# Optimization experiments

Measured on AMD Instinct MI355X. Metric: run time of the kernel, lower is better.

The kernel has to match this reference:

```python
import jax, jax.numpy as jnp
import numpy as np

NEG_SLOPE = 0.2
EPS = 1e-16  # PyG softmax eps


def gat_layer(x, edge_index, W_lin, b_lin, W_attn, b_attn):
    # GATConv: add self loops, x = lin(x), per-edge attention, segment softmax over
    # target nodes (edge_index[1]), scatter-add of x_j * alpha.
    N = x.shape[0]
    loops = jnp.arange(N, dtype=edge_index.dtype)
    src = jnp.concatenate([edge_index[0], loops])  # j (source / neighbor)
    dst = jnp.concatenate([edge_index[1], loops])  # i (target)
    x = x @ W_lin.T + b_lin                        # [N, D]
    D = x.shape[1]
    xi = x[dst]                                    # [E, D]
    xj = x[src]                                    # [E, D]
    # attn(cat(x_i, x_j)) split to avoid materializing the [E, 2D] concat
    Wi, Wj = W_attn[:, :D], W_attn[:, D:]
    alpha = xi @ Wi.T + xj @ Wj.T + b_attn         # [E, D]
    alpha = jax.nn.leaky_relu(alpha, NEG_SLOPE)
    # numerically stable segment softmax grouped by dst (per output channel)
    m = jax.ops.segment_max(alpha, dst, num_segments=N)
    alpha = jnp.exp(alpha - m[dst])
    denom = jax.ops.segment_sum(alpha, dst, num_segments=N)
    alpha = alpha / (denom[dst] + EPS)
    return jax.ops.segment_sum(xj * alpha, dst, num_segments=N)


def setup_inputs() -> dict:
    key = jax.random.key(0)
    ks = jax.random.split(key, 22)
    B, L, NN, E = 64, 50, 500, 256000
    EMB, D = 128, 128
    N = B * NN
    w = lambda k, shape: jax.random.normal(k, shape, jnp.float32) * 0.05
    return {
        "x": jax.random.normal(ks[0], (N, EMB), jnp.float32),
        "edge_index_0": jax.random.randint(ks[1], (2, E), 0, N, jnp.int32),
        "edge_index_1": jax.random.randint(ks[2], (2, E), 0, N, jnp.int32),
        "state_": jax.random.normal(ks[3], (B, D), jnp.float32),
        "input_": jax.random.normal(ks[4], (B, L, EMB), jnp.float32),
        "W_in": w(ks[5], (D, EMB)),
        "W_z": w(ks[6], (D, 2 * D)),
        "W_r": w(ks[7], (D, 2 * D)),
        "W_h": w(ks[8], (D, 2 * D)),
        "g0_Wlin": w(ks[9], (D, EMB)),
        "g0_blin": w(ks[10], (D,)),
        "g0_Wattn": w(ks[11], (D, 2 * D)),
        "g0_battn": w(ks[12], (D,)),
        "g1_Wlin": w(ks[13], (D, D)),
        "g1_blin": w(ks[14], (D,)),
        "g1_Wattn": w(ks[15], (D, 2 * D)),
        "g1_battn": w(ks[16], (D,)),
        "Wp": w(ks[17], (1, D)),
        "bp": w(ks[18], (1,)),
        "Ws": w(ks[19], (1, D)),
        "bs": w(ks[20], (1,)),
    }


def reference(x, edge_index_0, edge_index_1, state_, input_,
              W_in, W_z, W_r, W_h,
              g0_Wlin, g0_blin, g0_Wattn, g0_battn,
              g1_Wlin, g1_blin, g1_Wattn, g1_battn,
              Wp, bp, Ws, bs):
    B, D = state_.shape
    n_nodes = x.shape[0] // B
    # GRU-style gate on global state
    inp = jnp.mean(input_ @ W_in.T, axis=1)                 # [B, D]
    zi = jnp.concatenate([state_, inp], axis=-1)            # [B, 2D]
    z = jax.nn.sigmoid(zi @ W_z.T)
    r = jax.nn.sigmoid(zi @ W_r.T)
    h = jnp.tanh(jnp.concatenate([r * state_, inp], -1) @ W_h.T)
    h = (1 - z) * state_ + z * h                            # [B, D]
    # two GAT layers
    g0 = gat_layer(x, edge_index_0, g0_Wlin, g0_blin, g0_Wattn, g0_battn)
    g1 = gat_layer(g0, edge_index_1, g1_Wlin, g1_blin, g1_Wattn, g1_battn)
    xg = g1.reshape(B, n_nodes, D) * h[:, None, :]          # broadcast gate
    prob = (xg @ Wp.T + bp).reshape(B, n_nodes)
    sisr = jax.nn.sigmoid((xg @ Ws.T + bs).reshape(B, n_nodes))
    prob = jax.nn.softmax(prob[:, 1:], axis=-1)             # drop depot node 0
    return prob, sisr, h
```

## Files before the change

### kernel.cpp

```cpp
#include <hip/hip_runtime.h>
#include <math.h>

#define CAP  32
#define CAPB 4096
#define PART_CHUNK 4096

typedef __attribute__((ext_vector_type(8))) short bfrag;
typedef __attribute__((ext_vector_type(4))) float ffrag;
typedef __attribute__((ext_vector_type(2))) float f2v;

__device__ __forceinline__ float sigmoidf_(float x){ return 1.f/(1.f+__expf(-x)); }

__device__ __forceinline__ unsigned short f2bf(float f){
    unsigned u = __float_as_uint(f);
    u += 0x7fffu + ((u >> 16) & 1u);
    return (unsigned short)(u >> 16);
}
__device__ __forceinline__ float bf2f(unsigned u){
    return __uint_as_float((u & 0xffffu) << 16);
}

__global__ __launch_bounds__(256) void prep_kernel(
    const int* __restrict__ ei0, const int* __restrict__ ei1,
    int* __restrict__ binCnt, unsigned* __restrict__ bins, int E, int nA, int nb,
    const float* __restrict__ Wlin0, const float* __restrict__ Wattn0,
    const float* __restrict__ blin0, const float* __restrict__ battn0,
    const float* __restrict__ Wlin1, const float* __restrict__ Wattn1,
    const float* __restrict__ blin1, const float* __restrict__ battn1,
    unsigned short* __restrict__ wc, float* __restrict__ bc,
    const float* __restrict__ state_, const float* __restrict__ input_,
    const float* __restrict__ W_in, const float* __restrict__ W_z,
    const float* __restrict__ W_r, const float* __restrict__ W_h,
    float* __restrict__ h_out, int L)
{
    int blk = blockIdx.x;
    if (blk < 2 * nA) {
        __shared__ int lcnt[128];
        __shared__ int gbase[128];
        int g = (blk >= nA) ? 1 : 0;
        const int* ei = g ? ei1 : ei0;
        int base = (blk - g * nA) * PART_CHUNK;
        int tid = threadIdx.x;
        for (int t = tid; t < nb; t += 256) lcnt[t] = 0;
        __syncthreads();
        int lpos[16], binv[16]; unsigned wrd[16];
        #pragma unroll
        for (int i = 0; i < 16; ++i) {
            int e = base + i * 256 + tid;
            if (e < E) {
                int d = ei[E + e];
                int s = ei[e];
                int b = d >> 8;
                binv[i] = b;
                wrd[i]  = ((unsigned)(d & 255) << 24) | (unsigned)s;
                lpos[i] = atomicAdd(&lcnt[b], 1);
            } else binv[i] = -1;
        }
        __syncthreads();
        if (tid < nb) gbase[tid] = atomicAdd(&binCnt[g * nb + tid], lcnt[tid]);
        __syncthreads();
        #pragma unroll
        for (int i = 0; i < 16; ++i) {
            if (binv[i] >= 0) {
                int pos = gbase[binv[i]] + lpos[i];
                if (pos < CAPB) bins[(size_t)(g * nb + binv[i]) * CAPB + pos] = wrd[i];
            }
        }
    } else if (blk < 2 * nA + 387) {
        int idx = (blk - 2 * nA) * 256 + threadIdx.x;
        if (idx < 2 * 384 * 128) {
            int layer = idx / 49152;
            int t = idx - layer * 49152;
            int n = t >> 7, k = t & 127;
            const float* Wlin  = layer ? Wlin1  : Wlin0;
            const float* Wattn = layer ? Wattn1 : Wattn0;
            float v;
            if (n < 128) {
                v = Wlin[n * 128 + k];
            } else {
                int rr = (n < 256) ? (n - 128) : (n - 256);
                int off = (n < 256) ? 0 : 128;
                float s = 0.f;
                for (int d = 0; d < 128; ++d) s += Wattn[rr * 256 + off + d] * Wlin[d * 128 + k];
                v = s;
            }
            wc[idx] = f2bf(v);
        } else if (idx < 2 * 384 * 128 + 768) {
            int bi = idx - 2 * 384 * 128;
            int layer = bi / 384;
            int n = bi - layer * 384;
            const float* blin  = layer ? blin1  : blin0;
            const float* Wattn = layer ? Wattn1 : Wattn0;
            const float* battn = layer ? battn1 : battn0;
            float v;
            if (n < 128) v = blin[n];
            else {
                int rr = (n < 256) ? (n - 128) : (n - 256);
                int off = (n < 256) ? 0 : 128;
                float s = 0.f;
                for (int d = 0; d < 128; ++d) s += Wattn[rr * 256 + off + d] * blin[d];
                v = (n < 256) ? (s + battn[rr]) : s;
            }
            bc[bi] = v;
        }
    } else {
        __shared__ float wt[128 * 65];
        __shared__ float mu[128], ziv[256], zi2[256], zzv[128], stv[128];
        int tid = threadIdx.x;
        int b = blk - (2 * nA + 387);

        if (tid < 128) {
            float s = 0.f;
            const float* ip = input_ + (size_t)b * L * 128 + tid;
            #pragma unroll 5
            for (int l = 0; l < L; ++l) s += ip[(size_t)l * 128];
            mu[tid] = s / (float)L;
            float st = state_[b * 128 + tid];
            stv[tid] = st;
            ziv[tid] = st;
        }
        __syncthreads();

        #define LOADTILE(W, ldk, k0) { \
            _Pragma("unroll") \
            for (int j = 0; j < 8; ++j) { \
                int f = tid + 256 * j;                  \
                int row = f >> 4, c4 = (f & 15) << 2; \
                float4 v = *(const float4*)((W) + (size_t)row * (ldk) + (k0) + c4); \
                float* wp = &wt[row * 65 + c4]; \
                wp[0] = v.x; wp[1] = v.y; wp[2] = v.z; wp[3] = v.w; \
            } }
        #define GEMVT(vec, k0, acc) { \
            if (tid < 128) { \
                const float* wr_ = &wt[tid * 65]; \
                _Pragma("unroll") \
                for (int c = 0; c < 64; ++c) acc += wr_[c] * (vec)[(k0) + c]; \
            } }

        float accI = 0.f;
        LOADTILE(W_in, 128, 0);  __syncthreads(); GEMVT(mu, 0, accI);  __syncthreads();
        LOADTILE(W_in, 128, 64); __syncthreads(); GEMVT(mu, 64, accI); __syncthreads();
        if (tid < 128) ziv[128 + tid] = accI;
        __syncthreads();

        float accZ = 0.f;
        #pragma unroll
        for (int t4 = 0; t4 < 4; ++t4) {
            LOADTILE(W_z, 256, t4 * 64); __syncthreads();
            GEMVT(ziv, t4 * 64, accZ);   __syncthreads();
        }
        float accR = 0.f;
        #pragma unroll
        for (int t4 = 0; t4 < 4; ++t4) {
            LOADTILE(W_r, 256, t4 * 64); __syncthreads();
            GEMVT(ziv, t4 * 64, accR);   __syncthreads();
        }
        if (tid < 128) {
            float z = sigmoidf_(accZ), r = sigmoidf_(accR);
            zzv[tid] = z;
            zi2[tid] = r * stv[tid];
            zi2[128 + tid] = ziv[128 + tid];
        }
        __syncthreads();
        float accH = 0.f;
        #pragma unroll
        for (int t4 = 0; t4 < 4; ++t4) {
            LOADTILE(W_h, 256, t4 * 64); __syncthreads();
            GEMVT(zi2, t4 * 64, accH);   __syncthreads();
        }
        if (tid < 128) {
            float hc = tanhf(accH);
            float z = zzv[tid], st = stv[tid];
            h_out[b * 128 + tid] = (1.f - z) * st + z * hc;
        }
        #undef LOADTILE
        #undef GEMVT
    }
}

__global__ __launch_bounds__(256) void gemm384(const short* __restrict__ Xb, const float* __restrict__ Xf,
                                               const short* __restrict__ Wc, const float* __restrict__ bc,
                                               unsigned short* __restrict__ aib, unsigned short* __restrict__ pair,
                                               const unsigned* __restrict__ bins, const int* __restrict__ binCnt,
                                               int* __restrict__ cnt, unsigned short* __restrict__ esrc,
                                               int N, int nb, int gemmBlks)
{
    __shared__ __align__(16) char smem[384 * 40 * 2];
    if ((int)blockIdx.x >= gemmBlks) {
        int* cl = (int*)smem;
        unsigned short* el = (unsigned short*)(smem + 1024);
        int p = blockIdx.x - gemmBlks;
        int g = (p >= nb) ? 1 : 0;
        int bin = p - g * nb;
        int tid = threadIdx.x;
        cl[tid] = 0;
        __syncthreads();
        int m = binCnt[g * nb + bin]; if (m > CAPB) m = CAPB;
        const unsigned* bp_ = bins + (size_t)(g * nb + bin) * CAPB;
        for (int i = tid; i < m; i += 256) {
            unsigned w = bp_[i];
            int dl = (int)(w >> 24);
            int pp = atomicAdd(&cl[dl], 1);
            if (pp < CAP) el[dl * CAP + pp] = (unsigned short)w;
        }
        __syncthreads();
        int nodeBase = bin * 256;
        int* cg = cnt + (size_t)g * N;
        if (nodeBase + tid < N) cg[nodeBase + tid] = cl[tid];
        uint4* eo = (uint4*)(esrc + ((size_t)g * N + nodeBase) * CAP);
        const uint4* es = (const uint4*)el;
        #pragma unroll
        for (int k = 0; k < 4; ++k) eo[k * 256 + tid] = es[k * 256 + tid];
        return;
    }
    short* wlds = (short*)smem;
    int tid = threadIdx.x;
    int lane = tid & 63, wave = tid >> 6;
    int quad = lane >> 4, l16 = lane & 15;
    int mrow = blockIdx.x * 64 + wave * 16 + l16;

    bfrag av[4];
    if (Xf) {
        #pragma unroll
        for (int kk = 0; kk < 4; ++kk) {
            const float* xfp = Xf + (size_t)mrow * 128 + quad * 8 + kk * 32;
            float4 a0 = *(const float4*)(xfp);
            float4 a1 = *(const float4*)(xfp + 4);
            av[kk] = (bfrag){ (short)f2bf(a0.x), (short)f2bf(a0.y), (short)f2bf(a0.z), (short)f2bf(a0.w),
                              (short)f2bf(a1.x), (short)f2bf(a1.y), (short)f2bf(a1.z), (short)f2bf(a1.w) };
        }
    } else {
        #pragma unroll
        for (int kk = 0; kk < 4; ++kk)
            av[kk] = *(const bfrag*)(Xb + (size_t)mrow * 128 + quad * 8 + kk * 32);
    }

    ffrag acc[24];
    #pragma unroll
    for (int t = 0; t < 24; ++t) acc[t] = (ffrag){0.f, 0.f, 0.f, 0.f};

    #pragma unroll
    for (int kk = 0; kk < 4; ++kk) {
        __syncthreads();
        #pragma unroll
        for (int it = 0; it < 6; ++it) {
            int slot = it * 256 + tid;
            int row = slot >> 2, ch = slot & 3;
            *(bfrag*)&wlds[row * 40 + ch * 8] = *(const bfrag*)(Wc + (size_t)row * 128 + kk * 32 + ch * 8);
        }
        __syncthreads();
        #pragma unroll
        for (int t = 0; t < 24; ++t) {
            bfrag bv = *(const bfrag*)&wlds[(t * 16 + l16) * 40 + quad * 8];
            acc[t] = __builtin_amdgcn_mfma_f32_16x16x32_bf16(av[kk], bv, acc[t], 0, 0, 0);
        }
    }
    int rbase = blockIdx.x * 64 + wave * 16 + quad * 4;
    #pragma unroll
    for (int t = 0; t < 8; ++t) {
        int c = t * 16 + l16;
        float by = bc[c], bi = bc[128 + c], bj = bc[256 + c];
        #pragma unroll
        for (int r = 0; r < 4; ++r) {
            size_t off = (size_t)(rbase + r) * 128 + c;
            float yv  = acc[t][r]      + by;
            float aiv = acc[8 + t][r]  + bi;
            float ajv = acc[16 + t][r] + bj;
            aib[off] = f2bf(aiv);
            int w = __builtin_amdgcn_cvt_pk_fp8_f32(yv, ajv, 0, false);
            pair[off] = (unsigned short)w;
        }
    }
}

__global__ void aggregate_kernel(const unsigned short* __restrict__ aib, const unsigned* __restrict__ pair,
                                 const int* __restrict__ cnt, const unsigned short* __restrict__ esrc,
                                 unsigned* __restrict__ gb_out,
                                 const float* __restrict__ h, const float* __restrict__ Wp, const float* __restrict__ bp,
                                 const float* __restrict__ Ws, const float* __restrict__ bs,
                                 float* __restrict__ pbuf, float* __restrict__ sisr_out,
                                 int N, int NN, int fuse_score)
{
    int node = blockIdx.x * (blockDim.x >> 6) + (threadIdx.x >> 6);
    if (node >= N) return;
    int lane = threadIdx.x & 63;
    int c = 2 * lane;
    unsigned ain2 = *(const unsigned*)(aib + ((size_t)node << 7) + c);
    float ain0 = bf2f(ain2), ain1 = bf2f(ain2 >> 16);
    int deg = cnt[node]; if (deg > CAP) deg = CAP;
    const unsigned short* ep = esrc + (size_t)node * CAP;
    int myidx = (lane < deg) ? (int)ep[lane] : 0;

    float w0 = 0.f, w1 = 0.f, o0 = 0.f, o1 = 0.f;
    #define PROC(q) { \
        f2v lo = __builtin_amdgcn_cvt_pk_f32_fp8((int)(q), false); \
        f2v hi = __builtin_amdgcn_cvt_pk_f32_fp8((int)(q), true); \
        float a0 = ain0 + lo.y; \
        float a1 = ain1 + hi.y; \
        a0 = (a0 > 0.f) ? a0 : 0.2f * a0; \
        a1 = (a1 > 0.f) ? a1 : 0.2f * a1; \
        float e0 = __expf(a0), e1 = __expf(a1); \
        w0 += e0; w1 += e1; \
        o0 += e0 * lo.x; o1 += e1 * hi.x; }

    unsigned qs = pair[((size_t)node << 6) + lane];
    PROC(qs)

    int j = 0;
    for (; j + 8 <= deg; j += 8) {
        int s0 = __shfl(myidx, j),     s1 = __shfl(myidx, j + 1);
        int s2 = __shfl(myidx, j + 2), s3 = __shfl(myidx, j + 3);
        int s4 = __shfl(myidx, j + 4), s5 = __shfl(myidx, j + 5);
        int s6 = __shfl(myidx, j + 6), s7 = __shfl(myidx, j + 7);
        unsigned q0 = pair[((size_t)s0 << 6) + lane];
        unsigned q1 = pair[((size_t)s1 << 6) + lane];
        unsigned q2 = pair[((size_t)s2 << 6) + lane];
        unsigned q3 = pair[((size_t)s3 << 6) + lane];
        unsigned q4 = pair[((size_t)s4 << 6) + lane];
        unsigned q5 = pair[((size_t)s5 << 6) + lane];
        unsigned q6 = pair[((size_t)s6 << 6) + lane];
        unsigned q7 = pair[((size_t)s7 << 6) + lane];
        PROC(q0) PROC(q1) PROC(q2) PROC(q3) PROC(q4) PROC(q5) PROC(q6) PROC(q7)
    }
    if (j + 4 <= deg) {
        int s0 = __shfl(myidx, j),     s1 = __shfl(myidx, j + 1);
        int s2 = __shfl(myidx, j + 2), s3 = __shfl(myidx, j + 3);
        unsigned q0 = pair[((size_t)s0 << 6) + lane];
        unsigned q1 = pair[((size_t)s1 << 6) + lane];
        unsigned q2 = pair[((size_t)s2 << 6) + lane];
        unsigned q3 = pair[((size_t)s3 << 6) + lane];
        PROC(q0) PROC(q1) PROC(q2) PROC(q3)
        j += 4;
    }
    for (; j < deg; ++j) {
        int s0 = __shfl(myidx, j);
        unsigned q0 = pair[((size_t)s0 << 6) + lane];
        PROC(q0)
    }
    #undef PROC

    float g0 = o0 / (w0 + 1e-16f), g1 = o1 / (w1 + 1e-16f);
    if (!fuse_score) {
        gb_out[(size_t)node * 64 + lane] = (unsigned)f2bf(g0) | ((unsigned)f2bf(g1) << 16);
    } else {
        int b = node / NN;
        float xg0 = g0 * h[b * 128 + c], xg1 = g1 * h[b * 128 + c + 1];
        float pp = xg0 * Wp[c] + xg1 * Wp[c + 1];
        float ss = xg0 * Ws[c] + xg1 * Ws[c + 1];
        #pragma unroll
        for (int o = 32; o > 0; o >>= 1) { pp += __shfl_xor(pp, o); ss += __shfl_xor(ss, o); }
        if (lane == 0) {
            pbuf[node] = pp + bp[0];
            sisr_out[node] = sigmoidf_(ss + bs[0]);
        }
    }
}

__global__ void softmax_kernel(const float* __restrict__ pbuf, float* __restrict__ prob_out, int NN){
    int b = blockIdx.x, tid = threadIdx.x;
    __shared__ float sdata[512];
    bool valid = (tid >= 1 && tid < NN);
    float v = valid ? pbuf[b * NN + tid] : -INFINITY;
    sdata[tid] = v; __syncthreads();
    for (int o = 256; o > 0; o >>= 1) { if (tid < o) sdata[tid] = fmaxf(sdata[tid], sdata[tid + o]); __syncthreads(); }
    float m = sdata[0]; __syncthreads();
    float e = valid ? __expf(v - m) : 0.f;
    sdata[tid] = e; __syncthreads();
    for (int o = 256; o > 0; o >>= 1) { if (tid < o) sdata[tid] += sdata[tid + o]; __syncthreads(); }
    float ssum = sdata[0];
    if (valid) prob_out[(size_t)b * (NN - 1) + tid - 1] = e / ssum;
}

extern "C" void kernel_launch(void* const* d_in, const int* in_sizes, int n_in,
                              void* d_out, int out_size, void* d_ws, size_t ws_size,
                              hipStream_t stream)
{
    const float* x       = (const float*)d_in[0];
    const int*   ei0     = (const int*)d_in[1];
    const int*   ei1     = (const int*)d_in[2];
    const float* state_  = (const float*)d_in[3];
    const float* input_  = (const float*)d_in[4];
    const float* W_in    = (const float*)d_in[5];
    const float* W_z     = (const float*)d_in[6];
    const float* W_r     = (const float*)d_in[7];
    const float* W_h     = (const float*)d_in[8];
    const float* g0_Wlin = (const float*)d_in[9];
    const float* g0_blin = (const float*)d_in[10];
    const float* g0_Wattn= (const float*)d_in[11];
    const float* g0_battn= (const float*)d_in[12];
    const float* g1_Wlin = (const float*)d_in[13];
    const float* g1_blin = (const float*)d_in[14];
    const float* g1_Wattn= (const float*)d_in[15];
    const float* g1_battn= (const float*)d_in[16];
    const float* Wp      = (const float*)d_in[17];
    const float* bp      = (const float*)d_in[18];
    const float* Ws      = (const float*)d_in[19];
    const float* bs      = (const float*)d_in[20];

    const int N  = in_sizes[0] / 128;
    const int E  = in_sizes[1] / 2;
    const int B  = in_sizes[3] / 128;
    const int L  = in_sizes[4] / (B * 128);
    const int NN = N / B;
    const int nb = N >> 8;

    float* out      = (float*)d_out;
    float* prob_out = out;
    float* sisr_out = out + (size_t)B * (NN - 1);
    float* h_out    = sisr_out + (size_t)B * NN;

    unsigned short* aib = (unsigned short*)d_ws;
    unsigned* gbb  = (unsigned*)(aib + (size_t)N * 128);
    unsigned short* pair = (unsigned short*)(gbb + (size_t)N * 64);
    unsigned short* wc = pair + (size_t)N * 128;
    float* bc   = (float*)(wc + 2 * 384 * 128);
    float* pbuf = bc + 768;
    int* cnt0  = (int*)(pbuf + N);
    int* cnt1  = cnt0 + N;
    unsigned short* esrc0 = (unsigned short*)(cnt1 + N);
    unsigned short* esrc1 = esrc0 + (size_t)N * CAP;
    unsigned* bins = (unsigned*)(esrc1 + (size_t)N * CAP);
    int* binCnt = (int*)(bins + (size_t)2 * nb * CAPB);

    hipMemsetAsync(binCnt, 0, (size_t)2 * nb * sizeof(int), stream);

    const int nA = (E + PART_CHUNK - 1) / PART_CHUNK;
    prep_kernel<<<2 * nA + 387 + B, 256, 0, stream>>>(
        ei0, ei1, binCnt, bins, E, nA, nb,
        g0_Wlin, g0_Wattn, g0_blin, g0_battn,
        g1_Wlin, g1_Wattn, g1_blin, g1_battn,
        wc, bc,
        state_, input_, W_in, W_z, W_r, W_h, h_out, L);

    const int gemmBlks = N / 64;

    gemm384<<<gemmBlks + 2 * nb, 256, 0, stream>>>(nullptr, x, (const short*)wc, bc, aib, pair,
                                                   bins, binCnt, cnt0, esrc0, N, nb, gemmBlks);

    aggregate_kernel<<<(N + 3) / 4, 256, 0, stream>>>(aib, (const unsigned*)pair, cnt0, esrc0, gbb,
                                                      nullptr, nullptr, nullptr, nullptr, nullptr,
                                                      nullptr, nullptr, N, NN, 0);

    gemm384<<<gemmBlks, 256, 0, stream>>>((const short*)gbb, nullptr, (const short*)(wc + 49152), bc + 384, aib, pair,
                                          nullptr, nullptr, nullptr, nullptr, N, nb, gemmBlks);

    aggregate_kernel<<<(N + 3) / 4, 256, 0, stream>>>(aib, (const unsigned*)pair, cnt1, esrc1, nullptr,
                                                      h_out, Wp, bp, Ws, bs,
                                                      pbuf, sisr_out, N, NN, 1);

    softmax_kernel<<<B, 512, 0, stream>>>(pbuf, prob_out, NN);
}
```

Baseline: 207.0 us.

## Split aggregate wave into two half-waves processing alternate edges with 8-byte loads

Each 64-lane wave in the aggregation kernel now splits into two 32-lane halves. Each half handles every other neighbor edge with 4 channels per lane using uint2 loads, and the partial softmax sums are combined with a cross-half shuffle at the end. Up to eight neighbor rows are gathered up front before any processing, to raise memory-level parallelism in the random gather. The price is a final reduction step and more registers, and lanes idle when the degree is odd.

Measured after the change: 208.9 us. Within noise of the previous version (+0.9%).

```diff
diff --git a/kernel.cpp b/kernel.cpp
--- a/kernel.cpp
+++ b/kernel.cpp
@@ -124,7 +124,7 @@
         #define LOADTILE(W, ldk, k0) { \
             _Pragma("unroll") \
             for (int j = 0; j < 8; ++j) { \
-                int f = tid + 256 * j;                  \
+                int f = tid + 256 * j; \
                 int row = f >> 4, c4 = (f & 15) << 2; \
                 float4 v = *(const float4*)((W) + (size_t)row * (ldk) + (k0) + c4); \
                 float* wp = &wt[row * 65 + c4]; \
@@ -284,71 +284,88 @@
     int node = blockIdx.x * (blockDim.x >> 6) + (threadIdx.x >> 6);
     if (node >= N) return;
     int lane = threadIdx.x & 63;
-    int c = 2 * lane;
-    unsigned ain2 = *(const unsigned*)(aib + ((size_t)node << 7) + c);
-    float ain0 = bf2f(ain2), ain1 = bf2f(ain2 >> 16);
+    int half = lane >> 5, l32 = lane & 31;
+    int c0 = l32 << 2;
+
+    uint2 ainv = *(const uint2*)(aib + ((size_t)node << 7) + c0);
+    float a0 = bf2f(ainv.x), a1 = bf2f(ainv.x >> 16);
+    float a2 = bf2f(ainv.y), a3 = bf2f(ainv.y >> 16);
+
     int deg = cnt[node]; if (deg > CAP) deg = CAP;
+    int total = deg + 1;
     const unsigned short* ep = esrc + (size_t)node * CAP;
     int myidx = (lane < deg) ? (int)ep[lane] : 0;
 
-    float w0 = 0.f, w1 = 0.f, o0 = 0.f, o1 = 0.f;
-    #define PROC(q) { \
-        f2v lo = __builtin_amdgcn_cvt_pk_f32_fp8((int)(q), false); \
-        f2v hi = __builtin_amdgcn_cvt_pk_f32_fp8((int)(q), true); \
-        float a0 = ain0 + lo.y; \
-        float a1 = ain1 + hi.y; \
-        a0 = (a0 > 0.f) ? a0 : 0.2f * a0; \
-        a1 = (a1 > 0.f) ? a1 : 0.2f * a1; \
-        float e0 = __expf(a0), e1 = __expf(a1); \
-        w0 += e0; w1 += e1; \
-        o0 += e0 * lo.x; o1 += e1 * hi.x; }
-
-    unsigned qs = pair[((size_t)node << 6) + lane];
-    PROC(qs)
-
-    int j = 0;
-    for (; j + 8 <= deg; j += 8) {
-        int s0 = __shfl(myidx, j),     s1 = __shfl(myidx, j + 1);
-        int s2 = __shfl(myidx, j + 2), s3 = __shfl(myidx, j + 3);
-        int s4 = __shfl(myidx, j + 4), s5 = __shfl(myidx, j + 5);
-        int s6 = __shfl(myidx, j + 6), s7 = __shfl(myidx, j + 7);
-        unsigned q0 = pair[((size_t)s0 << 6) + lane];
-        unsigned q1 = pair[((size_t)s1 << 6) + lane];
-        unsigned q2 = pair[((size_t)s2 << 6) + lane];
-        unsigned q3 = pair[((size_t)s3 << 6) + lane];
-        unsigned q4 = pair[((size_t)s4 << 6) + lane];
-        unsigned q5 = pair[((size_t)s5 << 6) + lane];
-        unsigned q6 = pair[((size_t)s6 << 6) + lane];
-        unsigned q7 = pair[((size_t)s7 << 6) + lane];
-        PROC(q0) PROC(q1) PROC(q2) PROC(q3) PROC(q4) PROC(q5) PROC(q6) PROC(q7)
-    }
-    if (j + 4 <= deg) {
-        int s0 = __shfl(myidx, j),     s1 = __shfl(myidx, j + 1);
-        int s2 = __shfl(myidx, j + 2), s3 = __shfl(myidx, j + 3);
-        unsigned q0 = pair[((size_t)s0 << 6) + lane];
-        unsigned q1 = pair[((size_t)s1 << 6) + lane];
-        unsigned q2 = pair[((size_t)s2 << 6) + lane];
-        unsigned q3 = pair[((size_t)s3 << 6) + lane];
-        PROC(q0) PROC(q1) PROC(q2) PROC(q3)
-        j += 4;
-    }
-    for (; j < deg; ++j) {
-        int s0 = __shfl(myidx, j);
-        unsigned q0 = pair[((size_t)s0 << 6) + lane];
-        PROC(q0)
-    }
-    #undef PROC
+    float w0=0.f,w1=0.f,w2=0.f,w3=0.f, o0=0.f,o1=0.f,o2=0.f,o3=0.f;
+    const uint2* pr = (const uint2*)pair;
+
+    #define PROC4(q) { \
+        f2v p0 = __builtin_amdgcn_cvt_pk_f32_fp8((int)((q).x), false); \
+        f2v p1 = __builtin_amdgcn_cvt_pk_f32_fp8((int)((q).x), true);  \
+        f2v p2 = __builtin_amdgcn_cvt_pk_f32_fp8((int)((q).y), false); \
+        f2v p3 = __builtin_amdgcn_cvt_pk_f32_fp8((int)((q).y), true);  \
+        float t0 = a0 + p0.y, t1 = a1 + p1.y, t2 = a2 + p2.y, t3 = a3 + p3.y; \
+        t0 = (t0 > 0.f) ? t0 : 0.2f * t0; t1 = (t1 > 0.f) ? t1 : 0.2f * t1; \
+        t2 = (t2 > 0.f) ? t2 : 0.2f * t2; t3 = (t3 > 0.f) ? t3 : 0.2f * t3; \
+        float e0 = __expf(t0), e1 = __expf(t1), e2 = __expf(t2), e3 = __expf(t3); \
+        w0 += e0; w1 += e1; w2 += e2; w3 += e3; \
+        o0 += e0 * p0.x; o1 += e1 * p1.x; o2 += e2 * p2.x; o3 += e3 * p3.x; }
+
+    uint2 q0,q1,q2,q3,q4,q5,q6,q7;
+    {
+        int k, kk, sv, s;
+        #define ISSUE(i, qv) \
+            k = 2*(i) + half; \
+            if (k < total) { \
+                kk = (k > 0) ? (k - 1) : 0; \
+                sv = __shfl(myidx, kk); \
+                s  = (k == 0) ? node : sv; \
+                qv = pr[((size_t)s << 5) + l32]; \
+            }
+        ISSUE(0, q0) ISSUE(1, q1) ISSUE(2, q2) ISSUE(3, q3)
+        ISSUE(4, q4) ISSUE(5, q5) ISSUE(6, q6) ISSUE(7, q7)
+        #undef ISSUE
+    }
+    if (0 + half < total) PROC4(q0)
+    if (2 + half < total) PROC4(q1)
+    if (4 + half < total) PROC4(q2)
+    if (6 + half < total) PROC4(q3)
+    if (8 + half < total) PROC4(q4)
+    if (10 + half < total) PROC4(q5)
+    if (12 + half < total) PROC4(q6)
+    if (14 + half < total) PROC4(q7)
+    for (int k = 16 + half; k < total; k += 2) {
+        int sv = __shfl(myidx, k - 1);
+        uint2 q = pr[((size_t)sv << 5) + l32];
+        PROC4(q)
+    }
+    #undef PROC4
+
+    w0 += __shfl_xor(w0, 32); w1 += __shfl_xor(w1, 32);
+    w2 += __shfl_xor(w2, 32); w3 += __shfl_xor(w3, 32);
+    o0 += __shfl_xor(o0, 32); o1 += __shfl_xor(o1, 32);
+    o2 += __shfl_xor(o2, 32); o3 += __shfl_xor(o3, 32);
 
     float g0 = o0 / (w0 + 1e-16f), g1 = o1 / (w1 + 1e-16f);
+    float g2 = o2 / (w2 + 1e-16f), g3 = o3 / (w3 + 1e-16f);
+
     if (!fuse_score) {
-        gb_out[(size_t)node * 64 + lane] = (unsigned)f2bf(g0) | ((unsigned)f2bf(g1) << 16);
+        if (half == 0) {
+            uint2 outv;
+            outv.x = (unsigned)f2bf(g0) | ((unsigned)f2bf(g1) << 16);
+            outv.y = (unsigned)f2bf(g2) | ((unsigned)f2bf(g3) << 16);
+            *(uint2*)(gb_out + (size_t)node * 64 + 2 * l32) = outv;
+        }
     } else {
         int b = node / NN;
-        float xg0 = g0 * h[b * 128 + c], xg1 = g1 * h[b * 128 + c + 1];
-        float pp = xg0 * Wp[c] + xg1 * Wp[c + 1];
-        float ss = xg0 * Ws[c] + xg1 * Ws[c + 1];
-        #pragma unroll
-        for (int o = 32; o > 0; o >>= 1) { pp += __shfl_xor(pp, o); ss += __shfl_xor(ss, o); }
+        float4 hv = *(const float4*)(h + b * 128 + c0);
+        float4 wp = *(const float4*)(Wp + c0);
+        float4 ws = *(const float4*)(Ws + c0);
+        float xg0 = g0 * hv.x, xg1 = g1 * hv.y, xg2 = g2 * hv.z, xg3 = g3 * hv.w;
+        float pp = xg0 * wp.x + xg1 * wp.y + xg2 * wp.z + xg3 * wp.w;
+        float ss = xg0 * ws.x + xg1 * ws.y + xg2 * ws.z + xg3 * ws.w;
+        #pragma unroll
+        for (int o = 16; o > 0; o >>= 1) { pp += __shfl_xor(pp, o); ss += __shfl_xor(ss, o); }
         if (lane == 0) {
             pbuf[node] = pp + bp[0];
             sisr_out[node] = sigmoidf_(ss + bs[0]);
```
